# Performance work log

Measured on AMD Instinct MI355X. Metric: run time of the kernel, lower is better.

## Reference

```python
import jax, jax.numpy as jnp
import numpy as np

D_MODEL = 1024
N_HEADS = 16
D_K = D_MODEL // N_HEADS


def setup_inputs() -> dict:
    key = jax.random.key(0)
    ks = jax.random.split(key, 6)
    B, S = 4, 2048
    x = jax.random.normal(ks[0], (B, S, D_MODEL), dtype=jnp.float32)
    # nn.Linear weights are [out, in]; kept in that layout, applied as x @ W.T
    lim = 1.0 / np.sqrt(D_MODEL)
    w_q = jax.random.uniform(ks[1], (D_MODEL, D_MODEL), jnp.float32, -lim, lim)
    w_k = jax.random.uniform(ks[2], (D_MODEL, D_MODEL), jnp.float32, -lim, lim)
    w_v = jax.random.uniform(ks[3], (D_MODEL, D_MODEL), jnp.float32, -lim, lim)
    w_o = jax.random.uniform(ks[4], (D_MODEL, D_MODEL), jnp.float32, -lim, lim)
    b_o = jax.random.uniform(ks[5], (D_MODEL,), jnp.float32, -lim, lim)
    return {"x": x, "w_q": w_q, "w_k": w_k, "w_v": w_v, "w_o": w_o, "b_o": b_o}


def reference(x, w_q, w_k, w_v, w_o, b_o):
    B, S, _ = x.shape
    scale = 1.0 / np.sqrt(D_K).astype(np.float32)

    def split_heads(t):  # [B,S,D] -> [B,H,S,d_k]
        return t.reshape(B, S, N_HEADS, D_K).transpose(0, 2, 1, 3)

    q = split_heads(x @ w_q.T)
    k = split_heads(x @ w_k.T)
    v = split_heads(x @ w_v.T)

    scores = jnp.einsum('bhqd,bhkd->bhqk', q, k) * scale
    causal = jnp.tril(jnp.ones((S, S), dtype=bool))
    scores = jnp.where(causal[None, None], scores, -jnp.inf)
    attn = jax.nn.softmax(scores, axis=-1)  # dropout p=0 -> identity
    out = jnp.einsum('bhqk,bhkd->bhqd', attn, v)
    out = out.transpose(0, 2, 1, 3).reshape(B, S, D_MODEL)
    return out @ w_o.T + b_o
```

## Files before the change

kernel.cpp:

```cpp
#include <hip/hip_runtime.h>

typedef unsigned short ushort_t;
typedef __attribute__((ext_vector_type(8))) short short8;
typedef __attribute__((ext_vector_type(4))) float floatx4;


__device__ __forceinline__ ushort_t f2bf(float f) {
    unsigned int u = __float_as_uint(f);
    u = (u + 0x7FFFu + ((u >> 16) & 1u)) >> 16;
    return (ushort_t)u;
}

typedef __attribute__((address_space(1))) void gls_g;
typedef __attribute__((address_space(3))) void gls_l;

__device__ __forceinline__ void async_copy16(const ushort_t* g, ushort_t* l) {
    __builtin_amdgcn_global_load_lds((gls_g*)g, (gls_l*)l, 16, 0, 0);
}

__device__ __forceinline__ floatx4 mfma16(short8 a, short8 b, floatx4 c) {
    return __builtin_amdgcn_mfma_f32_16x16x32_bf16(a, b, c, 0, 0, 0);
}


__global__ __launch_bounds__(256) void conv_all(const float* __restrict__ x,
                                                const float* __restrict__ wq,
                                                const float* __restrict__ wk,
                                                const float* __restrict__ wv,
                                                const float* __restrict__ wo,
                                                ushort_t* __restrict__ xb,
                                                ushort_t* __restrict__ wqkv,
                                                ushort_t* __restrict__ wob) {
    const int bid = blockIdx.x;
    const float* in;
    ushort_t* out;
    int blk;
    if (bid < 8192) { in = x; out = xb; blk = bid; }
    else {
        const int g = (bid - 8192) >> 10;
        blk = (bid - 8192) & 1023;
        in  = (g == 0) ? wq : (g == 1) ? wk : (g == 2) ? wv : wo;
        out = (g == 3) ? wob : wqkv + g * 1048576;
    }
    const int i = (blk * 256 + threadIdx.x) * 4;
    float4 f = *(const float4*)(in + i);
    ushort4 o;
    o.x = f2bf(f.x); o.y = f2bf(f.y); o.z = f2bf(f.z); o.w = f2bf(f.w);
    *(ushort4*)(out + i) = o;
}


template<int BF16_OUT>
__global__ __launch_bounds__(256, 2) void gemm_nt(const ushort_t* __restrict__ A,
                                                  const ushort_t* __restrict__ B,
                                                  void* __restrict__ Cv,
                                                  const float* __restrict__ bias,
                                                  int M, int N, int K, int ldc) {
    __shared__ ushort_t lA[128 * 64];
    __shared__ ushort_t lB[128 * 64];
    const int tid  = threadIdx.x;
    const int wave = tid >> 6, lane = tid & 63;
    const int quad = lane >> 4, l15 = lane & 15;
    const int wr = (wave >> 1) * 64;
    const int wc = (wave & 1) * 64;
    const size_t bm = blockIdx.y, bn = blockIdx.x;

    const ushort_t* Ab = A + bm * 128 * (size_t)K;
    const ushort_t* Bb = B + bn * 128 * (size_t)K;

    int srow[4], scol[4];
#pragma unroll
    for (int i = 0; i < 4; ++i) {
        const int li = i * 256 + tid;
        srow[i] = li >> 3;
        scol[i] = ((li & 7) ^ (srow[i] & 7)) * 8;
    }

    floatx4 acc[4][4];
#pragma unroll
    for (int i = 0; i < 4; ++i)
#pragma unroll
        for (int j = 0; j < 4; ++j) acc[i][j] = (floatx4){0.f, 0.f, 0.f, 0.f};

    for (int kt = 0; kt < K; kt += 64) {
        __syncthreads();
#pragma unroll
        for (int i = 0; i < 4; ++i) {
            async_copy16(Ab + (size_t)srow[i] * K + kt + scol[i],
                         &lA[i * 2048] + wave * 512);
            async_copy16(Bb + (size_t)srow[i] * K + kt + scol[i],
                         &lB[i * 2048] + wave * 512);
        }
        __syncthreads();

        short8 af[4][2], bf[4][2];
#pragma unroll
        for (int mt = 0; mt < 4; ++mt)
#pragma unroll
            for (int ks = 0; ks < 2; ++ks)
                af[mt][ks] = *(const short8*)&lA[(wr + mt * 16 + l15) * 64 +
                                                 (((ks * 4 + quad) ^ (l15 & 7)) * 8)];
#pragma unroll
        for (int nt = 0; nt < 4; ++nt)
#pragma unroll
            for (int ks = 0; ks < 2; ++ks)
                bf[nt][ks] = *(const short8*)&lB[(wc + nt * 16 + l15) * 64 +
                                                 (((ks * 4 + quad) ^ (l15 & 7)) * 8)];
#pragma unroll
        for (int mt = 0; mt < 4; ++mt)
#pragma unroll
            for (int nt = 0; nt < 4; ++nt) {
                acc[mt][nt] = mfma16(af[mt][0], bf[nt][0], acc[mt][nt]);
                acc[mt][nt] = mfma16(af[mt][1], bf[nt][1], acc[mt][nt]);
            }
    }

#pragma unroll
    for (int mt = 0; mt < 4; ++mt)
#pragma unroll
        for (int nt = 0; nt < 4; ++nt)
#pragma unroll
            for (int r = 0; r < 4; ++r) {
                const size_t m = bm * 128 + wr + mt * 16 + quad * 4 + r;
                const size_t n = bn * 128 + wc + nt * 16 + l15;
                const float v = acc[mt][nt][r];
                if (BF16_OUT)
                    ((ushort_t*)Cv)[m * (size_t)ldc + n] = f2bf(v);
                else
                    ((float*)Cv)[m * (size_t)ldc + n] = v + bias[n];
            }
}


__global__ __launch_bounds__(256) void transpose_v(const ushort_t* __restrict__ qkv,
                                                   ushort_t* __restrict__ vt) {
    const int bh = blockIdx.y, b = bh >> 4, h = bh & 15;
    const int st = blockIdx.x;
    const int t  = threadIdx.x;
    const int sl  = t >> 2;
    const int dv0 = (t & 3) * 16;
    const int s = st * 64 + sl;
    const ushort_t* src = qkv + (size_t)(b * 2048 + s) * 3072 + 2048 + h * 64 + dv0;
    ushort_t v[16];
    *(uint4*)&v[0] = *(const uint4*)src;
    *(uint4*)&v[8] = *(const uint4*)(src + 8);
    const int s_lo = s & 31;
    const int j = ((s_lo >> 2) & 3) * 8 + ((s_lo >> 4) & 1) * 4 + (s_lo & 3);
    ushort_t* dst = vt + (size_t)(bh * 64) * 2048 + (s & ~31) + j;
#pragma unroll
    for (int i = 0; i < 16; ++i) dst[(size_t)(dv0 + i) * 2048] = v[i];
}


__global__ __launch_bounds__(256, 2) void attn_fwd(const ushort_t* __restrict__ qkv,
                                                   const ushort_t* __restrict__ vt,
                                                   ushort_t* __restrict__ attn) {
    __shared__ ushort_t lK[2][2048];
    __shared__ ushort_t lV[2][2048];
    const int tid = threadIdx.x, wave = tid >> 6, lane = tid & 63;
    const int quad = lane >> 4, l15 = lane & 15;
    const int bh = blockIdx.x & 63;
    const int slot = blockIdx.x >> 6;
    const int b = bh >> 4, h = bh & 15;

    const ushort_t* qb = qkv + (size_t)b * 2048 * 3072 + h * 64;
    const ushort_t* kb = qb + 1024;
    const ushort_t* vb = vt + (size_t)(bh * 64) * 2048;

    const int krow = tid >> 3;
    const ushort_t* ksrc = kb + (size_t)krow * 3072 + ((tid & 7) ^ (krow & 7)) * 8;
    const int vrow = tid >> 2;
    const ushort_t* vsrc = vb + (size_t)vrow * 2048 +
                           ((tid & 3) ^ ((vrow ^ (vrow >> 2)) & 3)) * 8;
    ushort_t* kdst = &lK[0][0] + wave * 512;
    ushort_t* vdst = &lV[0][0] + wave * 512;

    const int vfc = (quad ^ ((l15 ^ (l15 >> 2)) & 3)) * 8;
    const float C = 0.18033688011112042f;

#pragma unroll 1
    for (int phase = 0; phase < 2; ++phase) {
        const int t = phase ? 63 - (slot * 4 + wave) : slot * 4 + wave;
        const int n = phase ? 64 - slot * 4 : slot * 4 + 4;
        const int q0 = t * 32;

        short8 qf[2][2];
#pragma unroll
        for (int mt = 0; mt < 2; ++mt)
#pragma unroll
            for (int ks = 0; ks < 2; ++ks)
                qf[mt][ks] = *(const short8*)(qb +
                    (size_t)(q0 + mt * 16 + l15) * 3072 + ks * 32 + quad * 8);

        floatx4 o[2][4];
        float l[2] = {0.f, 0.f};
#pragma unroll
        for (int mt = 0; mt < 2; ++mt)
#pragma unroll
            for (int d = 0; d < 4; ++d) o[mt][d] = (floatx4){0.f, 0.f, 0.f, 0.f};

        __syncthreads();
        async_copy16(ksrc, kdst);
        async_copy16(vsrc, vdst);

#pragma unroll 1
        for (int ti = 0; ti < n; ++ti) {
            __syncthreads();
            if (ti + 1 < n) {
                const int nb = (ti + 1) & 1;
                async_copy16(ksrc + (size_t)(ti + 1) * 98304, kdst + nb * 2048);
                async_copy16(vsrc + (ti + 1) * 32,            vdst + nb * 2048);
            }
            if (ti <= t) {
                const int buf = ti & 1;
                const ushort_t* Kb = &lK[buf][0];
                const ushort_t* Vb = &lV[buf][0];
                short8 kf[2][2], vf[4];
#pragma unroll
                for (int ksub = 0; ksub < 2; ++ksub)
#pragma unroll
                    for (int ks = 0; ks < 2; ++ks)
                        kf[ksub][ks] = *(const short8*)(Kb + (ksub * 16 + l15) * 64 +
                                           (((ks * 4 + quad) ^ (l15 & 7)) * 8));
#pragma unroll
                for (int d = 0; d < 4; ++d)
                    vf[d] = *(const short8*)(Vb + (d * 16 + l15) * 32 + vfc);

                const bool diag = (ti == t);
#pragma unroll
                for (int mt = 0; mt < 2; ++mt) {
                    const floatx4 z = {0.f, 0.f, 0.f, 0.f};
                    floatx4 s0 = mfma16(kf[0][0], qf[mt][0], z);
                    s0 = mfma16(kf[0][1], qf[mt][1], s0);
                    float p[8];
                    if (mt == 0 && diag) {
#pragma unroll
                        for (int r = 0; r < 4; ++r) {
                            p[r] = __builtin_amdgcn_exp2f(s0[r] * C);
                            if (quad * 4 + r > l15) p[r] = 0.f;
                            p[r + 4] = 0.f;
                        }
                    } else {
                        floatx4 s1 = mfma16(kf[1][0], qf[mt][0], z);
                        s1 = mfma16(kf[1][1], qf[mt][1], s1);
#pragma unroll
                        for (int r = 0; r < 4; ++r) {
                            p[r]     = __builtin_amdgcn_exp2f(s0[r] * C);
                            p[r + 4] = __builtin_amdgcn_exp2f(s1[r] * C);
                        }
                        if (diag) {
#pragma unroll
                            for (int r = 0; r < 4; ++r)
                                if (quad * 4 + r > l15) p[r + 4] = 0.f;
                        }
                    }
                    l[mt] += ((p[0] + p[1]) + (p[2] + p[3])) +
                             ((p[4] + p[5]) + (p[6] + p[7]));

                    union { unsigned u[4]; short8 s8; } pk;
#pragma unroll
                    for (int j = 0; j < 4; ++j)
                        pk.u[j] = __builtin_amdgcn_perm(__float_as_uint(p[2 * j + 1]),
                                                        __float_as_uint(p[2 * j]),
                                                        0x07060302u);
                    const short8 pb = pk.s8;
#pragma unroll
                    for (int d = 0; d < 4; ++d)
                        o[mt][d] = mfma16(vf[d], pb, o[mt][d]);
                }
            }
        }

#pragma unroll
        for (int mt = 0; mt < 2; ++mt) {
            float lt = l[mt];
            lt += __shfl_xor(lt, 16);
            lt += __shfl_xor(lt, 32);
            const float inv = 1.0f / lt;
            ushort_t* orow = attn + (size_t)(b * 2048 + q0 + mt * 16 + l15) * 1024 + h * 64;
#pragma unroll
            for (int d = 0; d < 4; ++d) {
                ushort4 ov;
                ov.x = f2bf(o[mt][d][0] * inv);
                ov.y = f2bf(o[mt][d][1] * inv);
                ov.z = f2bf(o[mt][d][2] * inv);
                ov.w = f2bf(o[mt][d][3] * inv);
                *(ushort4*)(orow + d * 16 + quad * 4) = ov;
            }
        }
    }
}


extern "C" void kernel_launch(void* const* d_in, const int* in_sizes, int n_in,
                              void* d_out, int out_size, void* d_ws, size_t ws_size,
                              hipStream_t stream) {
    const float* x  = (const float*)d_in[0];
    const float* wq = (const float*)d_in[1];
    const float* wk = (const float*)d_in[2];
    const float* wv = (const float*)d_in[3];
    const float* wo = (const float*)d_in[4];
    const float* bo = (const float*)d_in[5];

    char* ws = (char*)d_ws;
    ushort_t* xb   = (ushort_t*)(ws);
    ushort_t* wqkv = (ushort_t*)(ws + 16777216);
    ushort_t* wob  = (ushort_t*)(ws + 23068672);
    ushort_t* qkv  = (ushort_t*)(ws + 25165824);
    ushort_t* vtb  = (ushort_t*)(ws + 75497472);
    ushort_t* attn = xb;
    float* out = (float*)d_out;

    conv_all<<<12288, 256, 0, stream>>>(x, wq, wk, wv, wo, xb, wqkv, wob);

    gemm_nt<1><<<dim3(24, 64), 256, 0, stream>>>(xb, wqkv, qkv, nullptr,
                                                 8192, 3072, 1024, 3072);
    transpose_v<<<dim3(32, 64), 256, 0, stream>>>(qkv, vtb);
    attn_fwd<<<512, 256, 0, stream>>>(qkv, vtb, attn);
    gemm_nt<0><<<dim3(8, 64), 256, 0, stream>>>(attn, wob, out, bo,
                                                8192, 1024, 1024, 1024);
}
```

Measured before the change: 238.1 us.

## Fuse V transpose into QKV GEMM epilogue and widen attention key tiles to 64

The QKV GEMM now writes V directly in the transposed, permuted layout the attention kernel expects, which removes the separate transpose_v launch and its extra global round-trip. The attention kernel now stages 64-key K/V tiles per iteration instead of 32, halving the number of barriers and async-copy rounds. It handles the 32-row causal granularity with two score groups and per-group diagonal masking. This doubles LDS use per block and raises register pressure, and it replaces the old V LDS swizzle with the K-style XOR layout.

```diff
diff --git a/kernel.cpp b/kernel.cpp
--- a/kernel.cpp
+++ b/kernel.cpp
@@ -50,12 +50,13 @@
 }
 
 
-template<int BF16_OUT>
+template<int MODE>
 __global__ __launch_bounds__(256, 2) void gemm_nt(const ushort_t* __restrict__ A,
                                                   const ushort_t* __restrict__ B,
                                                   void* __restrict__ Cv,
                                                   const float* __restrict__ bias,
-                                                  int M, int N, int K, int ldc) {
+                                                  int M, int N, int K, int ldc,
+                                                  ushort_t* __restrict__ vt) {
     __shared__ ushort_t lA[128 * 64];
     __shared__ ushort_t lB[128 * 64];
     const int tid  = threadIdx.x;
@@ -115,48 +116,94 @@
             }
     }
 
-#pragma unroll
-    for (int mt = 0; mt < 4; ++mt)
-#pragma unroll
-        for (int nt = 0; nt < 4; ++nt)
-#pragma unroll
-            for (int r = 0; r < 4; ++r) {
-                const size_t m = bm * 128 + wr + mt * 16 + quad * 4 + r;
-                const size_t n = bn * 128 + wc + nt * 16 + l15;
-                const float v = acc[mt][nt][r];
-                if (BF16_OUT)
-                    ((ushort_t*)Cv)[m * (size_t)ldc + n] = f2bf(v);
-                else
-                    ((float*)Cv)[m * (size_t)ldc + n] = v + bias[n];
-            }
-}
-
-
-__global__ __launch_bounds__(256) void transpose_v(const ushort_t* __restrict__ qkv,
-                                                   ushort_t* __restrict__ vt) {
-    const int bh = blockIdx.y, b = bh >> 4, h = bh & 15;
-    const int st = blockIdx.x;
-    const int t  = threadIdx.x;
-    const int sl  = t >> 2;
-    const int dv0 = (t & 3) * 16;
-    const int s = st * 64 + sl;
-    const ushort_t* src = qkv + (size_t)(b * 2048 + s) * 3072 + 2048 + h * 64 + dv0;
-    ushort_t v[16];
-    *(uint4*)&v[0] = *(const uint4*)src;
-    *(uint4*)&v[8] = *(const uint4*)(src + 8);
-    const int s_lo = s & 31;
-    const int j = ((s_lo >> 2) & 3) * 8 + ((s_lo >> 4) & 1) * 4 + (s_lo & 3);
-    ushort_t* dst = vt + (size_t)(bh * 64) * 2048 + (s & ~31) + j;
-#pragma unroll
-    for (int i = 0; i < 16; ++i) dst[(size_t)(dv0 + i) * 2048] = v[i];
-}
-
+    if (MODE == 0) {
+#pragma unroll
+        for (int mt = 0; mt < 4; ++mt)
+#pragma unroll
+            for (int nt = 0; nt < 4; ++nt)
+#pragma unroll
+                for (int r = 0; r < 4; ++r) {
+                    const size_t m = bm * 128 + wr + mt * 16 + quad * 4 + r;
+                    const size_t n = bn * 128 + wc + nt * 16 + l15;
+                    ((float*)Cv)[m * (size_t)ldc + n] = acc[mt][nt][r] + bias[n];
+                }
+    } else if ((int)bn < 16) {
+#pragma unroll
+        for (int mt = 0; mt < 4; ++mt)
+#pragma unroll
+            for (int nt = 0; nt < 4; ++nt)
+#pragma unroll
+                for (int r = 0; r < 4; ++r) {
+                    const size_t m = bm * 128 + wr + mt * 16 + quad * 4 + r;
+                    const size_t n = bn * 128 + wc + nt * 16 + l15;
+                    ((ushort_t*)Cv)[m * (size_t)ldc + n] = f2bf(acc[mt][nt][r]);
+                }
+    } else {
+        const int hh = ((int)bn - 16) * 2 + (wc >> 6);
+        const int bb = (int)(bm >> 4);
+        const size_t srow_off = (bm & 15) * 128 + wr;
+#pragma unroll
+        for (int mt = 0; mt < 4; ++mt)
+#pragma unroll
+            for (int nt = 0; nt < 4; ++nt) {
+                ushort4 ov;
+                ov.x = f2bf(acc[mt][nt][0]);
+                ov.y = f2bf(acc[mt][nt][1]);
+                ov.z = f2bf(acc[mt][nt][2]);
+                ov.w = f2bf(acc[mt][nt][3]);
+                ushort_t* dst = vt +
+                    ((size_t)((bb * 16 + hh) * 64 + nt * 16 + l15)) * 2048 +
+                    srow_off + (mt >> 1) * 32 + (mt & 1) * 4 + quad * 8;
+                *(ushort4*)dst = ov;
+            }
+    }
+}
+
+
+__device__ __forceinline__ short8 score_group(const short8 (&kg)[2][2],
+                                              short8 qf0, short8 qf1,
+                                              int dmask, int mt,
+                                              int quad, int l15, float& lacc) {
+    const float C = 0.18033688011112042f;
+    const floatx4 z = {0.f, 0.f, 0.f, 0.f};
+    float p[8];
+    floatx4 s0 = mfma16(kg[0][0], qf0, z);
+    s0 = mfma16(kg[0][1], qf1, s0);
+    if (dmask && mt == 0) {
+#pragma unroll
+        for (int r = 0; r < 4; ++r) {
+            p[r] = __builtin_amdgcn_exp2f(s0[r] * C);
+            if (quad * 4 + r > l15) p[r] = 0.f;
+            p[r + 4] = 0.f;
+        }
+    } else {
+        floatx4 s1 = mfma16(kg[1][0], qf0, z);
+        s1 = mfma16(kg[1][1], qf1, s1);
+#pragma unroll
+        for (int r = 0; r < 4; ++r) {
+            p[r]     = __builtin_amdgcn_exp2f(s0[r] * C);
+            p[r + 4] = __builtin_amdgcn_exp2f(s1[r] * C);
+        }
+        if (dmask) {
+#pragma unroll
+            for (int r = 0; r < 4; ++r)
+                if (quad * 4 + r > l15) p[r + 4] = 0.f;
+        }
+    }
+    lacc += ((p[0] + p[1]) + (p[2] + p[3])) + ((p[4] + p[5]) + (p[6] + p[7]));
+    union { unsigned u[4]; short8 s8; } pk;
+#pragma unroll
+    for (int j = 0; j < 4; ++j)
+        pk.u[j] = __builtin_amdgcn_perm(__float_as_uint(p[2 * j + 1]),
+                                        __float_as_uint(p[2 * j]), 0x07060302u);
+    return pk.s8;
+}
 
 __global__ __launch_bounds__(256, 2) void attn_fwd(const ushort_t* __restrict__ qkv,
                                                    const ushort_t* __restrict__ vt,
                                                    ushort_t* __restrict__ attn) {
-    __shared__ ushort_t lK[2][2048];
-    __shared__ ushort_t lV[2][2048];
+    __shared__ ushort_t lK[2][4096];
+    __shared__ ushort_t lV[2][4096];
     const int tid = threadIdx.x, wave = tid >> 6, lane = tid & 63;
     const int quad = lane >> 4, l15 = lane & 15;
     const int bh = blockIdx.x & 63;
@@ -167,21 +214,19 @@
     const ushort_t* kb = qb + 1024;
     const ushort_t* vb = vt + (size_t)(bh * 64) * 2048;
 
-    const int krow = tid >> 3;
-    const ushort_t* ksrc = kb + (size_t)krow * 3072 + ((tid & 7) ^ (krow & 7)) * 8;
-    const int vrow = tid >> 2;
-    const ushort_t* vsrc = vb + (size_t)vrow * 2048 +
-                           ((tid & 3) ^ ((vrow ^ (vrow >> 2)) & 3)) * 8;
-    ushort_t* kdst = &lK[0][0] + wave * 512;
-    ushort_t* vdst = &lV[0][0] + wave * 512;
-
-    const int vfc = (quad ^ ((l15 ^ (l15 >> 2)) & 3)) * 8;
-    const float C = 0.18033688011112042f;
+    const int r0 = tid >> 3;
+    const int r1 = 32 + r0;
+    const int c0 = ((tid & 7) ^ (r0 & 7)) * 8;
+    const int kc0 = (quad ^ (l15 & 7)) * 8;
+    const int kc1 = ((4 + quad) ^ (l15 & 7)) * 8;
 
 #pragma unroll 1
     for (int phase = 0; phase < 2; ++phase) {
         const int t = phase ? 63 - (slot * 4 + wave) : slot * 4 + wave;
-        const int n = phase ? 64 - slot * 4 : slot * 4 + 4;
+        const int tmaxb = phase ? 63 - slot * 4 : slot * 4 + 3;
+        const int n64 = (tmaxb >> 1) + 1;
+        const int Td = t >> 1;
+        const int todd = t & 1;
         const int q0 = t * 32;
 
         short8 qf[2][2];
@@ -200,73 +245,66 @@
             for (int d = 0; d < 4; ++d) o[mt][d] = (floatx4){0.f, 0.f, 0.f, 0.f};
 
         __syncthreads();
-        async_copy16(ksrc, kdst);
-        async_copy16(vsrc, vdst);
+        async_copy16(kb + (size_t)r0 * 3072 + c0, &lK[0][0]    + wave * 512);
+        async_copy16(kb + (size_t)r1 * 3072 + c0, &lK[0][2048] + wave * 512);
+        async_copy16(vb + (size_t)r0 * 2048 + c0, &lV[0][0]    + wave * 512);
+        async_copy16(vb + (size_t)r1 * 2048 + c0, &lV[0][2048] + wave * 512);
 
 #pragma unroll 1
-        for (int ti = 0; ti < n; ++ti) {
+        for (int T = 0; T < n64; ++T) {
             __syncthreads();
-            if (ti + 1 < n) {
-                const int nb = (ti + 1) & 1;
-                async_copy16(ksrc + (size_t)(ti + 1) * 98304, kdst + nb * 2048);
-                async_copy16(vsrc + (ti + 1) * 32,            vdst + nb * 2048);
-            }
-            if (ti <= t) {
-                const int buf = ti & 1;
+            if (T + 1 < n64) {
+                const int nb = (T + 1) & 1;
+                const ushort_t* kn = kb + (size_t)(T + 1) * 196608;
+                const ushort_t* vn = vb + (T + 1) * 64;
+                async_copy16(kn + (size_t)r0 * 3072 + c0, &lK[nb][0]    + wave * 512);
+                async_copy16(kn + (size_t)r1 * 3072 + c0, &lK[nb][2048] + wave * 512);
+                async_copy16(vn + (size_t)r0 * 2048 + c0, &lV[nb][0]    + wave * 512);
+                async_copy16(vn + (size_t)r1 * 2048 + c0, &lV[nb][2048] + wave * 512);
+            }
+            if (T <= Td) {
+                const int buf = T & 1;
                 const ushort_t* Kb = &lK[buf][0];
                 const ushort_t* Vb = &lV[buf][0];
-                short8 kf[2][2], vf[4];
-#pragma unroll
-                for (int ksub = 0; ksub < 2; ++ksub)
-#pragma unroll
-                    for (int ks = 0; ks < 2; ++ks)
-                        kf[ksub][ks] = *(const short8*)(Kb + (ksub * 16 + l15) * 64 +
-                                           (((ks * 4 + quad) ^ (l15 & 7)) * 8));
+                const bool diagT = (T == Td);
+                const bool hasG1 = (T < Td) || todd;
+                const int g0m = (diagT && !todd) ? 1 : 0;
+                const int g1m = (diagT && todd) ? 1 : 0;
+
+                short8 k0[2][2], v0[4], k1[2][2], v1[4];
+#pragma unroll
+                for (int s = 0; s < 2; ++s) {
+                    k0[s][0] = *(const short8*)(Kb + (s * 16 + l15) * 64 + kc0);
+                    k0[s][1] = *(const short8*)(Kb + (s * 16 + l15) * 64 + kc1);
+                }
 #pragma unroll
                 for (int d = 0; d < 4; ++d)
-                    vf[d] = *(const short8*)(Vb + (d * 16 + l15) * 32 + vfc);
-
-                const bool diag = (ti == t);
+                    v0[d] = *(const short8*)(Vb + (d * 16 + l15) * 64 + kc0);
+                if (hasG1) {
+#pragma unroll
+                    for (int s = 0; s < 2; ++s) {
+                        k1[s][0] = *(const short8*)(Kb + ((2 + s) * 16 + l15) * 64 + kc0);
+                        k1[s][1] = *(const short8*)(Kb + ((2 + s) * 16 + l15) * 64 + kc1);
+                    }
+#pragma unroll
+                    for (int d = 0; d < 4; ++d)
+                        v1[d] = *(const short8*)(Vb + (d * 16 + l15) * 64 + kc1);
+                }
+
 #pragma unroll
                 for (int mt = 0; mt < 2; ++mt) {
-                    const floatx4 z = {0.f, 0.f, 0.f, 0.f};
-                    floatx4 s0 = mfma16(kf[0][0], qf[mt][0], z);
-                    s0 = mfma16(kf[0][1], qf[mt][1], s0);
-                    float p[8];
-                    if (mt == 0 && diag) {
-#pragma unroll
-                        for (int r = 0; r < 4; ++r) {
-                            p[r] = __builtin_amdgcn_exp2f(s0[r] * C);
-                            if (quad * 4 + r > l15) p[r] = 0.f;
-                            p[r + 4] = 0.f;
-                        }
-                    } else {
-                        floatx4 s1 = mfma16(kf[1][0], qf[mt][0], z);
-                        s1 = mfma16(kf[1][1], qf[mt][1], s1);
-#pragma unroll
-                        for (int r = 0; r < 4; ++r) {
-                            p[r]     = __builtin_amdgcn_exp2f(s0[r] * C);
-                            p[r + 4] = __builtin_amdgcn_exp2f(s1[r] * C);
-                        }
-                        if (diag) {
-#pragma unroll
-                            for (int r = 0; r < 4; ++r)
-                                if (quad * 4 + r > l15) p[r + 4] = 0.f;
-                        }
+                    const short8 pb0 = score_group(k0, qf[mt][0], qf[mt][1],
+                                                   g0m, mt, quad, l15, l[mt]);
+#pragma unroll
+                    for (int d = 0; d < 4; ++d)
+                        o[mt][d] = mfma16(v0[d], pb0, o[mt][d]);
+                    if (hasG1) {
+                        const short8 pb1 = score_group(k1, qf[mt][0], qf[mt][1],
+                                                       g1m, mt, quad, l15, l[mt]);
+#pragma unroll
+                        for (int d = 0; d < 4; ++d)
+                            o[mt][d] = mfma16(v1[d], pb1, o[mt][d]);
                     }
-                    l[mt] += ((p[0] + p[1]) + (p[2] + p[3])) +
-                             ((p[4] + p[5]) + (p[6] + p[7]));
-
-                    union { unsigned u[4]; short8 s8; } pk;
-#pragma unroll
-                    for (int j = 0; j < 4; ++j)
-                        pk.u[j] = __builtin_amdgcn_perm(__float_as_uint(p[2 * j + 1]),
-                                                        __float_as_uint(p[2 * j]),
-                                                        0x07060302u);
-                    const short8 pb = pk.s8;
-#pragma unroll
-                    for (int d = 0; d < 4; ++d)
-                        o[mt][d] = mfma16(vf[d], pb, o[mt][d]);
                 }
             }
         }
@@ -314,9 +352,8 @@
     conv_all<<<12288, 256, 0, stream>>>(x, wq, wk, wv, wo, xb, wqkv, wob);
 
     gemm_nt<1><<<dim3(24, 64), 256, 0, stream>>>(xb, wqkv, qkv, nullptr,
-                                                 8192, 3072, 1024, 3072);
-    transpose_v<<<dim3(32, 64), 256, 0, stream>>>(qkv, vtb);
+                                                 8192, 3072, 1024, 3072, vtb);
     attn_fwd<<<512, 256, 0, stream>>>(qkv, vtb, attn);
     gemm_nt<0><<<dim3(8, 64), 256, 0, stream>>>(attn, wob, out, bo,
-                                                8192, 1024, 1024, 1024);
-}
+                                                8192, 1024, 1024, 1024, nullptr);
+}
```

After: 228.1 us. 1.04x faster.
